# Optimization experiments

Measured on AMD Instinct MI355X. Metric: run time of the kernel, lower is better.

The kernel has to match this reference:

```python
import jax, jax.numpy as jnp
import numpy as np

N, C, MH, MW = 128, 256, 28, 28
K = 80          # num_classes
P = 196         # cfg.num_points
SH, SW = 200, 200  # stride-4 semantic feature map
STRIDE = 4.0
FC_IN = C + 2 * K  # 416


def _bilinear(feat, px, py):
    # feat: (C,H,W); px,py: (N,P) pixel coords. grid_sample semantics:
    # align_corners=False, zero padding.
    _, H, W = feat.shape
    x0 = jnp.floor(px); y0 = jnp.floor(py)
    wx1 = px - x0; wy1 = py - y0
    def corner(xc, yc, w):
        valid = (xc >= 0) & (xc <= W - 1) & (yc >= 0) & (yc <= H - 1)
        xi = jnp.clip(xc, 0, W - 1).astype(jnp.int32)
        yi = jnp.clip(yc, 0, H - 1).astype(jnp.int32)
        return feat[:, yi, xi] * (w * valid)[None]  # (C,N,P)
    out = (corner(x0, y0, (1 - wx1) * (1 - wy1)) + corner(x0 + 1, y0, wx1 * (1 - wy1))
           + corner(x0, y0 + 1, (1 - wx1) * wy1) + corner(x0 + 1, y0 + 1, wx1 * wy1))
    return jnp.transpose(out, (1, 0, 2))  # (N,C,P)


def setup_inputs():
    key = jax.random.key(0)
    ks = jax.random.split(key, 16)
    s = 0.02
    instance_feats = jax.random.normal(ks[0], (N, C, MH, MW), jnp.float32)
    semantic_feat = jax.random.normal(ks[1], (1, C, SH, SW), jnp.float32)
    img_w, img_h = SW * STRIDE, SH * STRIDE
    x1 = jax.random.uniform(ks[2], (N,)) * (img_w * 0.5)
    y1 = jax.random.uniform(ks[3], (N,)) * (img_h * 0.5)
    bw = 32.0 + jax.random.uniform(ks[4], (N,)) * (img_w * 0.4)
    bh = 32.0 + jax.random.uniform(ks[5], (N,)) * (img_h * 0.4)
    rois = jnp.stack([jnp.zeros((N,)), x1, y1,
                      jnp.minimum(x1 + bw, img_w - 1),
                      jnp.minimum(y1 + bh, img_h - 1)], axis=1)
    roi_labels = jax.random.randint(ks[6], (N,), 0, K)
    return dict(
        instance_feats=instance_feats, semantic_feat=semantic_feat, rois=rois,
        roi_labels=roi_labels, num_points=P,
        w_sem=s * jax.random.normal(ks[7], (C, C)), b_sem=jnp.zeros((C,)),
        w_inst=s * jax.random.normal(ks[8], (K, C)), b_inst=jnp.zeros((K,)),
        w_det=s * jax.random.normal(ks[9], (K, C)), b_det=jnp.zeros((K,)),
        fc_w0=s * jax.random.normal(ks[10], (C, FC_IN)), fc_b0=jnp.zeros((C,)),
        fc_w1=s * jax.random.normal(ks[11], (C, FC_IN)), fc_b1=jnp.zeros((C,)),
        fc_w2=s * jax.random.normal(ks[12], (C, FC_IN)), fc_b2=jnp.zeros((C,)),
        w_logits=s * jax.random.normal(ks[13], (C, FC_IN)), b_logits=jnp.zeros((C,)),
        w_fuse=s * jax.random.normal(ks[14], (C, C)), b_fuse=jnp.zeros((C,)))


def reference(instance_feats, semantic_feat, rois, roi_labels, num_points,
              w_sem, b_sem, w_inst, b_inst, w_det, b_det,
              fc_w0, fc_b0, fc_w1, fc_b1, fc_w2, fc_b2,
              w_logits, b_logits, w_fuse, b_fuse):
    n, c, mh, mw = instance_feats.shape
    hw = mh * mw
    sem = jax.nn.relu(jnp.einsum('bchw,oc->bohw', semantic_feat, w_sem) + b_sem[None, :, None, None])
    inst_log = jnp.einsum('nchw,oc->nohw', instance_feats, w_inst) + b_inst[None, :, None, None]
    det_log = jnp.einsum('nchw,oc->nohw', instance_feats, w_det) + b_det[None, :, None, None]
    ridx = jnp.arange(n)
    instance_preds = inst_log[ridx, roi_labels][:, None]  # (n,1,mh,mw) class-selected
    detail_preds = det_log[ridx, roi_labels][:, None]
    # top-k uncertain-point selection on the (detached) detail map
    point_map = jax.lax.stop_gradient(detail_preds.reshape(n, hw))
    _, point_indices = jax.lax.top_k(point_map, num_points)  # (n,P)
    rel_x = ((point_indices % mw).astype(jnp.float32) + 0.5) / mw
    rel_y = ((point_indices // mw).astype(jnp.float32) + 0.5) / mh
    # roi-relative [0,1]^2 -> semantic feature map pixel coords (align_corners=False)
    px = (rois[:, 1:2] + rel_x * (rois[:, 3:4] - rois[:, 1:2])) / STRIDE - 0.5
    py = (rois[:, 2:3] + rel_y * (rois[:, 4:5] - rois[:, 2:3])) / STRIDE - 0.5
    fine = _bilinear(sem[0], px, py)  # (n,C,P); all rois belong to image 0
    k = inst_log.shape[1]
    idx = jnp.broadcast_to(point_indices[:, None, :], (n, k, point_indices.shape[1]))
    c_inst = jnp.take_along_axis(inst_log.reshape(n, k, hw), idx, axis=2)  # (n,K,P)
    c_det = jnp.take_along_axis(det_log.reshape(n, k, hw), idx, axis=2)
    x = jnp.concatenate([fine, c_inst, c_det], axis=1)  # (n, C+2K, P)
    for w_, b_ in ((fc_w0, fc_b0), (fc_w1, fc_b1), (fc_w2, fc_b2)):
        x = jax.nn.relu(jnp.einsum('ncp,oc->nop', x, w_) + b_[None, :, None])
        x = jnp.concatenate([x, c_inst, c_det], axis=1)
    pts = jnp.einsum('ncp,oc->nop', x, w_logits) + b_logits[None, :, None]  # (n,C,P)
    coarse = instance_feats.reshape(n, c, hw)
    refined = coarse.at[ridx[:, None, None], jnp.arange(c)[None, :, None],
                        point_indices[:, None, :]].set(pts)
    refined = refined.reshape(n, c, mh, mw)
    fused = jax.nn.relu(jnp.einsum('nchw,oc->nohw', refined, w_fuse) + b_fuse[None, :, None, None])
    up = jax.image.resize(fused, (n, c, 2 * mh, 2 * mw), method='bilinear')
    return instance_preds, detail_preds, jax.nn.relu(up)
```

## Files before the change

kernel.cpp:

```cpp
#include <hip/hip_runtime.h>

#define NN   128
#define CC   256
#define MH   28
#define MW   28
#define HW   784
#define KCLS 80
#define PP   196
#define SHH  200
#define SWW  200
#define SPIX 40000
#define FCIN 416

typedef __attribute__((ext_vector_type(8))) short short8;
typedef __attribute__((ext_vector_type(4))) float f32x4;

__device__ __forceinline__ unsigned short f2bf(float x) {
  unsigned u = __float_as_uint(x);
  unsigned r = (u + 0x7fffu + ((u >> 16) & 1u)) >> 16;
  return (unsigned short)r;
}
__device__ __forceinline__ float bf2f(unsigned short h) {
  return __uint_as_float((unsigned)h << 16);
}

#define OW_SEM  0
#define OW_FUSE 65536
#define OW_FC0  131072
#define OW_FC1  237568
#define OW_FC2  344064
#define OW_LOG  450560
#define OW_CAT  557056
#define OW_TOT  598016
__global__ void wconv_k(const float* __restrict__ wsem, const float* __restrict__ wfuse,
                        const float* __restrict__ w0, const float* __restrict__ w1,
                        const float* __restrict__ w2, const float* __restrict__ wlog,
                        const float* __restrict__ wi, const float* __restrict__ wd,
                        const float* __restrict__ bi, const float* __restrict__ bd,
                        unsigned short* __restrict__ out, float* __restrict__ bcat) {
  const int tid0 = blockIdx.x * blockDim.x + threadIdx.x;
  if (tid0 < KCLS) bcat[tid0] = bi[tid0];
  else if (tid0 < 2 * KCLS) bcat[tid0] = bd[tid0 - KCLS];
  for (int i = tid0; i < OW_TOT; i += gridDim.x * blockDim.x) {
    float v;
    if (i < OW_FUSE) v = wsem[i];
    else if (i < OW_FC0) v = wfuse[i - OW_FUSE];
    else if (i < OW_FC1) v = w0[i - OW_FC0];
    else if (i < OW_FC2) v = w1[i - OW_FC1];
    else if (i < OW_LOG) v = w2[i - OW_FC2];
    else if (i < OW_CAT) v = wlog[i - OW_LOG];
    else if (i < OW_CAT + KCLS * 256) v = wi[i - OW_CAT];
    else v = wd[i - OW_CAT - KCLS * 256];
    out[i] = f2bf(v);
  }
}

__global__ __launch_bounds__(256) void transpose_bf16_k(
    const float* __restrict__ src, unsigned short* __restrict__ dst, int P) {
  __shared__ float T[64][69];
  const int t = threadIdx.x;
  src += (size_t)blockIdx.z * 256 * P;
  dst += (size_t)blockIdx.z * P * 256;
  const int p0 = blockIdx.x * 64, c0 = blockIdx.y * 64;
#pragma unroll
  for (int it = 0; it < 16; ++it) {
    int idx = it * 256 + t, c = idx >> 6, p = idx & 63;
    T[c][p] = (p0 + p < P) ? src[(size_t)(c0 + c) * P + p0 + p] : 0.f;
  }
  __syncthreads();
#pragma unroll
  for (int it = 0; it < 16; ++it) {
    int idx = it * 256 + t, p = idx >> 6, c = idx & 63;
    if (p0 + p < P) dst[(size_t)(p0 + p) * 256 + c0 + c] = f2bf(T[c][p]);
  }
}

template <int ASRC, int EPI>
__global__ __launch_bounds__(256) void gemm_mfma_k(
    const void* __restrict__ Ap, const unsigned short* __restrict__ Bmat,
    const float* __restrict__ bias, float* __restrict__ outf,
    unsigned short* __restrict__ outh, const int* __restrict__ pidx,
    int M, int N, int K, int lda, int ldb) {
  __shared__ __align__(16) unsigned short Abuf[128 * 40];
  __shared__ __align__(16) unsigned short Bbuf[128 * 40];
  const int t = threadIdx.x;
  const int m0 = blockIdx.x * 128, n0 = blockIdx.y * 128;
  if (EPI == 3) {
    Bmat += (size_t)blockIdx.z * HW * 256;
    outf += (size_t)blockIdx.z * CC * HW;
  }
  const unsigned short* Ah = (const unsigned short*)Ap;
  const int wave = t >> 6, lane = t & 63, lq = lane >> 4, lr = lane & 15;
  const int msub = (wave & 1) * 64, nsub = (wave >> 1) * 64;
  f32x4 acc[4][4] = {};
  for (int kc = 0; kc < K; kc += 32) {
#pragma unroll
    for (int it = 0; it < 4; ++it) {
      const int idx = it * 256 + t, r = idx >> 3, jg = idx & 7;
      const int gm = m0 + r;
      ushort4 h = make_ushort4(0, 0, 0, 0);
      if (ASRC == 1) {
        if (gm < M) h = *(const ushort4*)&Ah[(size_t)gm * lda + kc + jg * 4];
      } else {
        if (gm < M) {
          const int nimg = gm / PP;
          const int srow = pidx[gm];
          h = *(const ushort4*)&Ah[((size_t)nimg * HW + srow) * 256 + kc + jg * 4];
        }
      }
      *(ushort4*)&Abuf[r * 40 + jg * 4] = h;
    }
#pragma unroll
    for (int it = 0; it < 4; ++it) {
      const int idx = it * 256 + t, r = idx >> 3, jg = idx & 7;
      const int gn = n0 + r;
      ushort4 h = make_ushort4(0, 0, 0, 0);
      if (gn < N) h = *(const ushort4*)&Bmat[(size_t)gn * ldb + kc + jg * 4];
      *(ushort4*)&Bbuf[r * 40 + jg * 4] = h;
    }
    __syncthreads();
    short8 af[4], bfr[4];
#pragma unroll
    for (int i = 0; i < 4; ++i)
      af[i] = *(const short8*)&Abuf[(msub + i * 16 + lr) * 40 + lq * 8];
#pragma unroll
    for (int f = 0; f < 4; ++f)
      bfr[f] = *(const short8*)&Bbuf[(nsub + f * 16 + lr) * 40 + lq * 8];
#pragma unroll
    for (int i = 0; i < 4; ++i)
#pragma unroll
      for (int f = 0; f < 4; ++f)
        acc[i][f] = __builtin_amdgcn_mfma_f32_16x16x32_bf16(af[i], bfr[f],
                                                            acc[i][f], 0, 0, 0);
    __syncthreads();
  }
#pragma unroll
  for (int i = 0; i < 4; ++i) {
#pragma unroll
    for (int r = 0; r < 4; ++r) {
      const int gm = m0 + msub + i * 16 + lq * 4 + r;
      if (EPI == 0) {
        if (gm < M) {
#pragma unroll
          for (int f = 0; f < 4; ++f) {
            const int go = n0 + nsub + f * 16 + lr;
            outh[(size_t)gm * FCIN + go] = f2bf(fmaxf(acc[i][f][r] + bias[go], 0.f));
          }
        }
      } else if (EPI == 1) {
        if (gm < M) {
          const int nimg = gm / PP;
          const int sidx = pidx[gm];
          unsigned short* dst = outh + ((size_t)nimg * HW + sidx) * 256;
#pragma unroll
          for (int f = 0; f < 4; ++f) {
            const int go = n0 + nsub + f * 16 + lr;
            dst[go] = f2bf(acc[i][f][r] + bias[go]);
          }
        }
      } else if (EPI == 3) {
        const float bb = bias[gm];
#pragma unroll
        for (int f = 0; f < 4; ++f) {
          const int gs = n0 + nsub + f * 16 + lr;
          if (gs < N) outf[(size_t)gm * HW + gs] = fmaxf(acc[i][f][r] + bb, 0.f);
        }
      } else if (EPI == 4) {
        if (gm < M) {
#pragma unroll
          for (int f = 0; f < 4; ++f) {
            const int go = n0 + nsub + f * 16 + lr;
            outh[(size_t)gm * 256 + go] = f2bf(fmaxf(acc[i][f][r] + bias[go], 0.f));
          }
        }
      } else {
        if (gm < M) {
          unsigned short* dx = outh + (size_t)gm * FCIN + 256;
          unsigned short* dy = (unsigned short*)outf + (size_t)gm * FCIN + 256;
#pragma unroll
          for (int f = 0; f < 4; ++f) {
            const int go = n0 + nsub + f * 16 + lr;
            if (go < N) {
              const unsigned short v = f2bf(acc[i][f][r] + bias[go]);
              dx[go] = v;
              dy[go] = v;
            }
          }
        }
      }
    }
  }
}

__global__ __launch_bounds__(256) void select_maps_k(
    const float* __restrict__ inst, const int* __restrict__ labels,
    const float* __restrict__ w_inst, const float* __restrict__ b_inst,
    const float* __restrict__ w_det, const float* __restrict__ b_det,
    float* __restrict__ out0, float* __restrict__ out1) {
  const int n = blockIdx.x;
  const int s = blockIdx.y * 196 + threadIdx.x;
  if (threadIdx.x >= 196) return;
  const int lab = labels[n];
  const float* fi = inst + (size_t)n * CC * HW + s;
  const float* wi = w_inst + lab * 256;
  const float* wd = w_det + lab * 256;
  double ai = 0.0, ad = 0.0;
  for (int c = 0; c < 256; ++c) {
    const float v = fi[c * HW];
    ai += (double)v * (double)wi[c];
    ad += (double)v * (double)wd[c];
  }
  out0[n * HW + s] = (float)(ai + (double)b_inst[lab]);
  out1[n * HW + s] = (float)(ad + (double)b_det[lab]);
}

__global__ __launch_bounds__(256) void topk_k(const float* __restrict__ det,
                                              int* __restrict__ pidx) {
  __shared__ unsigned long long keys[1024];
  const int n = blockIdx.x;
  for (int i = threadIdx.x; i < 1024; i += 256) {
    unsigned long long kk = 0ull;
    if (i < HW) {
      unsigned u = __float_as_uint(det[n * HW + i]);
      u = (u & 0x80000000u) ? ~u : (u | 0x80000000u);
      kk = ((unsigned long long)u << 32) | (unsigned)(1023 - i);
    }
    keys[i] = kk;
  }
  __syncthreads();
  for (int k = 2; k <= 1024; k <<= 1) {
    for (int j = k >> 1; j > 0; j >>= 1) {
      for (int i = threadIdx.x; i < 1024; i += 256) {
        const int l = i ^ j;
        if (l > i) {
          const bool up = ((i & k) == 0);
          unsigned long long a = keys[i], bb = keys[l];
          if ((a > bb) == up) { keys[i] = bb; keys[l] = a; }
        }
      }
      __syncthreads();
    }
  }
  for (int r = threadIdx.x; r < PP; r += 256)
    pidx[n * PP + r] = 1023 - (int)(keys[828 + r] & 1023ull);
}

__global__ __launch_bounds__(256) void fine_sample_k(
    const unsigned short* __restrict__ sem, const int* __restrict__ pidx,
    const float* __restrict__ rois, unsigned short* __restrict__ X) {
  const int n = blockIdx.x;
  const int t = threadIdx.x;
  const int p = blockIdx.y * 8 + (t >> 5);
  const int c0 = (t & 31) * 8;
  if (p >= PP) return;
  const int idx = pidx[n * PP + p];
  const float rx = ((float)(idx % MW) + 0.5f) / (float)MW;
  const float ry = ((float)(idx / MW) + 0.5f) / (float)MH;
  const float x1 = rois[n * 5 + 1], y1 = rois[n * 5 + 2];
  const float x2 = rois[n * 5 + 3], y2 = rois[n * 5 + 4];
  const float px = (x1 + rx * (x2 - x1)) * 0.25f - 0.5f;
  const float py = (y1 + ry * (y2 - y1)) * 0.25f - 0.5f;
  const float x0f = floorf(px), y0f = floorf(py);
  const int x0 = (int)x0f, y0 = (int)y0f;
  const float wx1 = px - x0f, wy1 = py - y0f;
  float out[8] = {};
#pragma unroll
  for (int cy = 0; cy < 2; ++cy) {
    const int yy = y0 + cy;
    const bool vy = (yy >= 0) && (yy <= SHH - 1);
    const int yc = min(max(yy, 0), SHH - 1);
    const float wy = cy ? wy1 : (1.f - wy1);
#pragma unroll
    for (int cx = 0; cx < 2; ++cx) {
      const int xx = x0 + cx;
      const bool vx = (xx >= 0) && (xx <= SWW - 1);
      const int xc = min(max(xx, 0), SWW - 1);
      const float wgt = (vx && vy) ? wy * (cx ? wx1 : (1.f - wx1)) : 0.f;
      const unsigned short* src = sem + ((size_t)yc * SWW + xc) * 256 + c0;
      short8 v = *(const short8*)src;
#pragma unroll
      for (int j = 0; j < 8; ++j) out[j] += wgt * bf2f((unsigned short)v[j]);
    }
  }
  unsigned short* dst = X + ((size_t)n * PP + p) * FCIN + c0;
  short8 o;
#pragma unroll
  for (int j = 0; j < 8; ++j) o[j] = (short)f2bf(out[j]);
  *(short8*)dst = o;
}

__global__ __launch_bounds__(256) void upsample_k(const float* __restrict__ fused,
                                                  float* __restrict__ out2) {
  __shared__ float L[HW];
  const int n = blockIdx.x, c = blockIdx.y;
  const float* src = fused + ((size_t)n * CC + c) * HW;
  for (int i = threadIdx.x; i < HW; i += 256) L[i] = src[i];
  __syncthreads();
  float* dst = out2 + ((size_t)n * CC + c) * 3136;
  for (int i = threadIdx.x; i < 3136; i += 256) {
    const int r = i / 56, q = i % 56;
    const float y = fminf(fmaxf(r * 0.5f - 0.25f, 0.f), 27.f);
    const float x = fminf(fmaxf(q * 0.5f - 0.25f, 0.f), 27.f);
    const int y0 = (int)y, x0 = (int)x;
    const float wy1 = y - (float)y0, wx1 = x - (float)x0;
    const int y1 = min(y0 + 1, 27), x1 = min(x0 + 1, 27);
    const float v00 = L[y0 * 28 + x0], v01 = L[y0 * 28 + x1];
    const float v10 = L[y1 * 28 + x0], v11 = L[y1 * 28 + x1];
    const float v = (1.f - wy1) * ((1.f - wx1) * v00 + wx1 * v01) +
                    wy1 * ((1.f - wx1) * v10 + wx1 * v11);
    dst[i] = fmaxf(v, 0.f);
  }
}

extern "C" void kernel_launch(void* const* d_in, const int* in_sizes, int n_in,
                              void* d_out, int out_size, void* d_ws, size_t ws_size,
                              hipStream_t stream) {
  (void)in_sizes; (void)n_in; (void)out_size; (void)ws_size;
  const float* inst   = (const float*)d_in[0];
  const float* semf   = (const float*)d_in[1];
  const float* rois   = (const float*)d_in[2];
  const int*   labels = (const int*)d_in[3];
  const float* w_sem  = (const float*)d_in[5];
  const float* b_sem  = (const float*)d_in[6];
  const float* w_inst = (const float*)d_in[7];
  const float* b_inst = (const float*)d_in[8];
  const float* w_det  = (const float*)d_in[9];
  const float* b_det  = (const float*)d_in[10];
  const float* fc_w0  = (const float*)d_in[11];
  const float* fc_b0  = (const float*)d_in[12];
  const float* fc_w1  = (const float*)d_in[13];
  const float* fc_b1  = (const float*)d_in[14];
  const float* fc_w2  = (const float*)d_in[15];
  const float* fc_b2  = (const float*)d_in[16];
  const float* w_log  = (const float*)d_in[17];
  const float* b_log  = (const float*)d_in[18];
  const float* w_fuse = (const float*)d_in[19];
  const float* b_fuse = (const float*)d_in[20];

  float* out0 = (float*)d_out;
  float* out1 = out0 + NN * HW;
  float* out2 = out0 + 2 * NN * HW;

  float* ws = (float*)d_ws;
  float* fused               = ws;
  int*   pidx                = (int*)(ws + 25690112);
  unsigned short* semh       = (unsigned short*)(ws + 25715200);
  unsigned short* semf_t     = (unsigned short*)(ws + 30835200);
  unsigned short* Xh         = (unsigned short*)(ws + 35955200);
  unsigned short* Yh         = (unsigned short*)(ws + 41173504);
  unsigned short* refined_t  = (unsigned short*)(ws + 46391808);
  unsigned short* wbf        = (unsigned short*)(ws + 59236864);
  float* bcat                = ws + 59535872;

  wconv_k<<<512, 256, 0, stream>>>(w_sem, w_fuse, fc_w0, fc_w1, fc_w2, w_log,
                                   w_inst, w_det, b_inst, b_det, wbf, bcat);
  transpose_bf16_k<<<dim3(625, 4, 1), 256, 0, stream>>>(semf, semf_t, SPIX);
  gemm_mfma_k<1, 4><<<dim3(313, 2, 1), 256, 0, stream>>>(
      semf_t, wbf + OW_SEM, b_sem, nullptr, semh, nullptr, SPIX, 256, 256, 256, 256);
  transpose_bf16_k<<<dim3(13, 4, NN), 256, 0, stream>>>(inst, refined_t, HW);
  select_maps_k<<<dim3(NN, 4), 256, 0, stream>>>(inst, labels, w_inst, b_inst,
                                                 w_det, b_det, out0, out1);
  topk_k<<<NN, 256, 0, stream>>>(out1, pidx);
  gemm_mfma_k<2, 5><<<dim3(196, 2, 1), 256, 0, stream>>>(
      refined_t, wbf + OW_CAT, bcat, (float*)Yh, Xh, pidx, NN * PP, 160, 256, 256, 256);
  fine_sample_k<<<dim3(NN, 25), 256, 0, stream>>>(semh, pidx, rois, Xh);
  gemm_mfma_k<1, 0><<<dim3(196, 2, 1), 256, 0, stream>>>(
      Xh, wbf + OW_FC0, fc_b0, nullptr, Yh, nullptr, NN * PP, 256, FCIN, FCIN, FCIN);
  gemm_mfma_k<1, 0><<<dim3(196, 2, 1), 256, 0, stream>>>(
      Yh, wbf + OW_FC1, fc_b1, nullptr, Xh, nullptr, NN * PP, 256, FCIN, FCIN, FCIN);
  gemm_mfma_k<1, 0><<<dim3(196, 2, 1), 256, 0, stream>>>(
      Xh, wbf + OW_FC2, fc_b2, nullptr, Yh, nullptr, NN * PP, 256, FCIN, FCIN, FCIN);
  gemm_mfma_k<1, 1><<<dim3(196, 2, 1), 256, 0, stream>>>(
      Yh, wbf + OW_LOG, b_log, nullptr, refined_t, pidx, NN * PP, 256, FCIN, FCIN, FCIN);
  gemm_mfma_k<1, 3><<<dim3(2, 7, NN), 256, 0, stream>>>(
      wbf + OW_FUSE, refined_t, b_fuse, fused, nullptr, nullptr, 256, HW, 256, 256, 256);
  upsample_k<<<dim3(NN, CC), 256, 0, stream>>>(fused, out2);
}
```

Before: 1.000 ms.

## Fuse point-head gather, sampling and MLP chain into one kernel

Replaces the coarse-logit gather GEMM, the fine bilinear sampling kernel, the three FC layers and the logits GEMM with a single kernel. Each block owns 64 point rows and keeps the 416-wide activation row in shared memory across all four layers, scattering the final logits straight back into refined_t. This removes five launches and the global round-trips of the X/Y intermediates. In exchange, weights are read from global memory with no LDS staging, there are only 392 blocks, and each layer has two barriers.

```diff
diff --git a/kernel.cpp b/kernel.cpp
--- a/kernel.cpp
+++ b/kernel.cpp
@@ -99,15 +99,7 @@
       const int idx = it * 256 + t, r = idx >> 3, jg = idx & 7;
       const int gm = m0 + r;
       ushort4 h = make_ushort4(0, 0, 0, 0);
-      if (ASRC == 1) {
-        if (gm < M) h = *(const ushort4*)&Ah[(size_t)gm * lda + kc + jg * 4];
-      } else {
-        if (gm < M) {
-          const int nimg = gm / PP;
-          const int srow = pidx[gm];
-          h = *(const ushort4*)&Ah[((size_t)nimg * HW + srow) * 256 + kc + jg * 4];
-        }
-      }
+      if (gm < M) h = *(const ushort4*)&Ah[(size_t)gm * lda + kc + jg * 4];
       *(ushort4*)&Abuf[r * 40 + jg * 4] = h;
     }
 #pragma unroll
@@ -139,26 +131,7 @@
 #pragma unroll
     for (int r = 0; r < 4; ++r) {
       const int gm = m0 + msub + i * 16 + lq * 4 + r;
-      if (EPI == 0) {
-        if (gm < M) {
-#pragma unroll
-          for (int f = 0; f < 4; ++f) {
-            const int go = n0 + nsub + f * 16 + lr;
-            outh[(size_t)gm * FCIN + go] = f2bf(fmaxf(acc[i][f][r] + bias[go], 0.f));
-          }
-        }
-      } else if (EPI == 1) {
-        if (gm < M) {
-          const int nimg = gm / PP;
-          const int sidx = pidx[gm];
-          unsigned short* dst = outh + ((size_t)nimg * HW + sidx) * 256;
-#pragma unroll
-          for (int f = 0; f < 4; ++f) {
-            const int go = n0 + nsub + f * 16 + lr;
-            dst[go] = f2bf(acc[i][f][r] + bias[go]);
-          }
-        }
-      } else if (EPI == 3) {
+      if (EPI == 3) {
         const float bb = bias[gm];
 #pragma unroll
         for (int f = 0; f < 4; ++f) {
@@ -173,22 +146,147 @@
             outh[(size_t)gm * 256 + go] = f2bf(fmaxf(acc[i][f][r] + bias[go], 0.f));
           }
         }
-      } else {
-        if (gm < M) {
-          unsigned short* dx = outh + (size_t)gm * FCIN + 256;
-          unsigned short* dy = (unsigned short*)outf + (size_t)gm * FCIN + 256;
+      }
+    }
+  }
+}
+
+#define XRS 424
+__global__ __launch_bounds__(256) void fused_point_k(
+    const unsigned short* __restrict__ semh,
+    unsigned short* __restrict__ refined_t,
+    const int* __restrict__ pidx, const float* __restrict__ rois,
+    const unsigned short* __restrict__ wbf, const float* __restrict__ bcat,
+    const float* __restrict__ fb0, const float* __restrict__ fb1,
+    const float* __restrict__ fb2, const float* __restrict__ bl) {
+  __shared__ __align__(16) unsigned short X[64 * XRS];
+  __shared__ int rowoff[64];
+  __shared__ float pxs[64], pys[64];
+  const int t = threadIdx.x;
+  const int gm0 = blockIdx.x * 64;
+  const int lane = t & 63, wave = t >> 6, lq = lane >> 4, lr = lane & 15;
+  if (t < 64) {
+    const int gm = gm0 + t;
+    const int n = gm / PP;
+    const int si = pidx[gm];
+    rowoff[t] = (n * HW + si) * 256;
+    const float rx = ((float)(si % MW) + 0.5f) / (float)MW;
+    const float ry = ((float)(si / MW) + 0.5f) / (float)MH;
+    const float x1 = rois[n * 5 + 1], y1 = rois[n * 5 + 2];
+    const float x2 = rois[n * 5 + 3], y2 = rois[n * 5 + 4];
+    pxs[t] = (x1 + rx * (x2 - x1)) * 0.25f - 0.5f;
+    pys[t] = (y1 + ry * (y2 - y1)) * 0.25f - 0.5f;
+  }
+  __syncthreads();
+  {
+    const int c0 = (t & 31) * 8;
+    const int rbase = t >> 5;
+#pragma unroll
+    for (int it = 0; it < 8; ++it) {
+      const int r = it * 8 + rbase;
+      const float px = pxs[r], py = pys[r];
+      const float x0f = floorf(px), y0f = floorf(py);
+      const int x0 = (int)x0f, y0 = (int)y0f;
+      const float wx1 = px - x0f, wy1 = py - y0f;
+      float out[8] = {};
+#pragma unroll
+      for (int cy = 0; cy < 2; ++cy) {
+        const int yy = y0 + cy;
+        const bool vy = (yy >= 0) && (yy <= SHH - 1);
+        const int yc = min(max(yy, 0), SHH - 1);
+        const float wy = cy ? wy1 : (1.f - wy1);
+#pragma unroll
+        for (int cx = 0; cx < 2; ++cx) {
+          const int xx = x0 + cx;
+          const bool vx = (xx >= 0) && (xx <= SWW - 1);
+          const int xc = min(max(xx, 0), SWW - 1);
+          const float wgt = (vx && vy) ? wy * (cx ? wx1 : (1.f - wx1)) : 0.f;
+          const unsigned short* src = semh + ((size_t)yc * SWW + xc) * 256 + c0;
+          short8 v = *(const short8*)src;
+#pragma unroll
+          for (int j = 0; j < 8; ++j) out[j] += wgt * bf2f((unsigned short)v[j]);
+        }
+      }
+      short8 o;
+#pragma unroll
+      for (int j = 0; j < 8; ++j) o[j] = (short)f2bf(out[j]);
+      *(short8*)&X[r * XRS + c0] = o;
+    }
+  }
+  {
+    const int grow = rowoff[wave * 16 + lr];
+    const unsigned short* Wc = wbf + OW_CAT;
+    f32x4 acc[10] = {};
+    for (int kc = 0; kc < 256; kc += 32) {
+      const short8 a = *(const short8*)&refined_t[(size_t)grow + kc + lq * 8];
+#pragma unroll
+      for (int f = 0; f < 10; ++f) {
+        const short8 b = *(const short8*)&Wc[(size_t)(f * 16 + lr) * 256 + kc + lq * 8];
+        acc[f] = __builtin_amdgcn_mfma_f32_16x16x32_bf16(a, b, acc[f], 0, 0, 0);
+      }
+    }
+#pragma unroll
+    for (int f = 0; f < 10; ++f) {
+      const int col = 256 + f * 16 + lr;
+      const float bb = bcat[f * 16 + lr];
+#pragma unroll
+      for (int r = 0; r < 4; ++r) {
+        const int row = wave * 16 + lq * 4 + r;
+        X[row * XRS + col] = f2bf(acc[f][r] + bb);
+      }
+    }
+  }
+  __syncthreads();
+  const int n0w = wave * 64;
+  for (int layer = 0; layer < 4; ++layer) {
+    const unsigned short* Wl = wbf + OW_FC0 + layer * 106496;
+    const float* bias = (layer == 0) ? fb0 : (layer == 1) ? fb1
+                        : (layer == 2) ? fb2 : bl;
+    f32x4 acc[4][4] = {};
+#pragma unroll 2
+    for (int kc = 0; kc < FCIN; kc += 32) {
+      short8 af[4], bfr[4];
+#pragma unroll
+      for (int i = 0; i < 4; ++i)
+        af[i] = *(const short8*)&X[(i * 16 + lr) * XRS + kc + lq * 8];
+#pragma unroll
+      for (int f = 0; f < 4; ++f)
+        bfr[f] = *(const short8*)&Wl[(size_t)(n0w + f * 16 + lr) * FCIN + kc + lq * 8];
+#pragma unroll
+      for (int i = 0; i < 4; ++i)
+#pragma unroll
+        for (int f = 0; f < 4; ++f)
+          acc[i][f] = __builtin_amdgcn_mfma_f32_16x16x32_bf16(af[i], bfr[f],
+                                                              acc[i][f], 0, 0, 0);
+    }
+    __syncthreads();
+    if (layer < 3) {
+#pragma unroll
+      for (int i = 0; i < 4; ++i)
+#pragma unroll
+        for (int r = 0; r < 4; ++r) {
+          const int row = i * 16 + lq * 4 + r;
 #pragma unroll
           for (int f = 0; f < 4; ++f) {
-            const int go = n0 + nsub + f * 16 + lr;
-            if (go < N) {
-              const unsigned short v = f2bf(acc[i][f][r] + bias[go]);
-              dx[go] = v;
-              dy[go] = v;
-            }
+            const int col = n0w + f * 16 + lr;
+            X[row * XRS + col] = f2bf(fmaxf(acc[i][f][r] + bias[col], 0.f));
           }
         }
-      }
-    }
+    } else {
+#pragma unroll
+      for (int i = 0; i < 4; ++i)
+#pragma unroll
+        for (int r = 0; r < 4; ++r) {
+          const int row = i * 16 + lq * 4 + r;
+          unsigned short* dst = refined_t + (size_t)rowoff[row];
+#pragma unroll
+          for (int f = 0; f < 4; ++f) {
+            const int col = n0w + f * 16 + lr;
+            dst[col] = f2bf(acc[i][f][r] + bias[col]);
+          }
+        }
+    }
+    __syncthreads();
   }
 }
 
@@ -243,50 +341,6 @@
   }
   for (int r = threadIdx.x; r < PP; r += 256)
     pidx[n * PP + r] = 1023 - (int)(keys[828 + r] & 1023ull);
-}
-
-__global__ __launch_bounds__(256) void fine_sample_k(
-    const unsigned short* __restrict__ sem, const int* __restrict__ pidx,
-    const float* __restrict__ rois, unsigned short* __restrict__ X) {
-  const int n = blockIdx.x;
-  const int t = threadIdx.x;
-  const int p = blockIdx.y * 8 + (t >> 5);
-  const int c0 = (t & 31) * 8;
-  if (p >= PP) return;
-  const int idx = pidx[n * PP + p];
-  const float rx = ((float)(idx % MW) + 0.5f) / (float)MW;
-  const float ry = ((float)(idx / MW) + 0.5f) / (float)MH;
-  const float x1 = rois[n * 5 + 1], y1 = rois[n * 5 + 2];
-  const float x2 = rois[n * 5 + 3], y2 = rois[n * 5 + 4];
-  const float px = (x1 + rx * (x2 - x1)) * 0.25f - 0.5f;
-  const float py = (y1 + ry * (y2 - y1)) * 0.25f - 0.5f;
-  const float x0f = floorf(px), y0f = floorf(py);
-  const int x0 = (int)x0f, y0 = (int)y0f;
-  const float wx1 = px - x0f, wy1 = py - y0f;
-  float out[8] = {};
-#pragma unroll
-  for (int cy = 0; cy < 2; ++cy) {
-    const int yy = y0 + cy;
-    const bool vy = (yy >= 0) && (yy <= SHH - 1);
-    const int yc = min(max(yy, 0), SHH - 1);
-    const float wy = cy ? wy1 : (1.f - wy1);
-#pragma unroll
-    for (int cx = 0; cx < 2; ++cx) {
-      const int xx = x0 + cx;
-      const bool vx = (xx >= 0) && (xx <= SWW - 1);
-      const int xc = min(max(xx, 0), SWW - 1);
-      const float wgt = (vx && vy) ? wy * (cx ? wx1 : (1.f - wx1)) : 0.f;
-      const unsigned short* src = sem + ((size_t)yc * SWW + xc) * 256 + c0;
-      short8 v = *(const short8*)src;
-#pragma unroll
-      for (int j = 0; j < 8; ++j) out[j] += wgt * bf2f((unsigned short)v[j]);
-    }
-  }
-  unsigned short* dst = X + ((size_t)n * PP + p) * FCIN + c0;
-  short8 o;
-#pragma unroll
-  for (int j = 0; j < 8; ++j) o[j] = (short)f2bf(out[j]);
-  *(short8*)dst = o;
 }
 
 __global__ __launch_bounds__(256) void upsample_k(const float* __restrict__ fused,
@@ -346,11 +400,9 @@
   int*   pidx                = (int*)(ws + 25690112);
   unsigned short* semh       = (unsigned short*)(ws + 25715200);
   unsigned short* semf_t     = (unsigned short*)(ws + 30835200);
-  unsigned short* Xh         = (unsigned short*)(ws + 35955200);
-  unsigned short* Yh         = (unsigned short*)(ws + 41173504);
-  unsigned short* refined_t  = (unsigned short*)(ws + 46391808);
-  unsigned short* wbf        = (unsigned short*)(ws + 59236864);
-  float* bcat                = ws + 59535872;
+  unsigned short* refined_t  = (unsigned short*)(ws + 35955200);
+  unsigned short* wbf        = (unsigned short*)(ws + 48800256);
+  float* bcat                = ws + 49099264;
 
   wconv_k<<<512, 256, 0, stream>>>(w_sem, w_fuse, fc_w0, fc_w1, fc_w2, w_log,
                                    w_inst, w_det, b_inst, b_det, wbf, bcat);
@@ -361,17 +413,8 @@
   select_maps_k<<<dim3(NN, 4), 256, 0, stream>>>(inst, labels, w_inst, b_inst,
                                                  w_det, b_det, out0, out1);
   topk_k<<<NN, 256, 0, stream>>>(out1, pidx);
-  gemm_mfma_k<2, 5><<<dim3(196, 2, 1), 256, 0, stream>>>(
-      refined_t, wbf + OW_CAT, bcat, (float*)Yh, Xh, pidx, NN * PP, 160, 256, 256, 256);
-  fine_sample_k<<<dim3(NN, 25), 256, 0, stream>>>(semh, pidx, rois, Xh);
-  gemm_mfma_k<1, 0><<<dim3(196, 2, 1), 256, 0, stream>>>(
-      Xh, wbf + OW_FC0, fc_b0, nullptr, Yh, nullptr, NN * PP, 256, FCIN, FCIN, FCIN);
-  gemm_mfma_k<1, 0><<<dim3(196, 2, 1), 256, 0, stream>>>(
-      Yh, wbf + OW_FC1, fc_b1, nullptr, Xh, nullptr, NN * PP, 256, FCIN, FCIN, FCIN);
-  gemm_mfma_k<1, 0><<<dim3(196, 2, 1), 256, 0, stream>>>(
-      Xh, wbf + OW_FC2, fc_b2, nullptr, Yh, nullptr, NN * PP, 256, FCIN, FCIN, FCIN);
-  gemm_mfma_k<1, 1><<<dim3(196, 2, 1), 256, 0, stream>>>(
-      Yh, wbf + OW_LOG, b_log, nullptr, refined_t, pidx, NN * PP, 256, FCIN, FCIN, FCIN);
+  fused_point_k<<<392, 256, 0, stream>>>(semh, refined_t, pidx, rois, wbf, bcat,
+                                         fc_b0, fc_b1, fc_b2, b_log);
   gemm_mfma_k<1, 3><<<dim3(2, 7, NN), 256, 0, stream>>>(
       wbf + OW_FUSE, refined_t, b_fuse, fused, nullptr, nullptr, 256, HW, 256, 256, 256);
   upsample_k<<<dim3(NN, CC), 256, 0, stream>>>(fused, out2);
```

Measured after the change: 845.9 us. -15.4%, faster.
